# Kernel tuning notes

Hardware: AMD Instinct MI355X
Metric: run time of the kernel (lower is better)

## Reference

```python
import jax, jax.numpy as jnp
import numpy as np

B, IN, OUT = 256, 1024, 1024


def choquet_cardinal(z):
    """Discrete Choquet integral over last axis with cardinality measure mu(A)=|A|/n.
    ChI(x) = sum_i (x_(i) - x_(i-1)) * mu(A_i), x_(0)=0, mu(A_i)=(n-i+1)/n.
    """
    n = z.shape[-1]
    xs = jnp.sort(z, axis=-1)  # ascending
    # diffs[..., 0] = x_(1); diffs[..., i] = x_(i+1) - x_(i)
    diffs = jnp.concatenate([xs[..., :1], jnp.diff(xs, axis=-1)], axis=-1)
    mu = (n - jnp.arange(n, dtype=xs.dtype)) / n  # 1, (n-1)/n, ..., 1/n
    return jnp.einsum('...i,i->...', diffs, mu)


def setup_inputs() -> dict:
    key = jax.random.key(0)
    kx, kw, kb = jax.random.split(key, 3)
    x = jax.random.normal(kx, (B, 1, IN), dtype=jnp.float32)
    weight = jax.random.normal(kw, (IN, OUT), dtype=jnp.float32) * 0.02
    bias = jax.random.normal(kb, (IN, OUT), dtype=jnp.float32) * 0.02
    return {"x": x, "weight": weight, "bias": bias}


def reference(x, weight, bias):
    # z: [B, OUT, IN] = x * W^T + b^T (elementwise with broadcast)
    z = x * weight.T + bias.T
    chi = choquet_cardinal(z)  # [B, OUT]
    return jax.nn.sigmoid(chi)
```

## Files before the change

kernel.cpp:

```cpp
#include <hip/hip_runtime.h>
#include <math.h>


#define BATCH   256
#define IN_DIM  1024
#define OUT_DIM 1024

#define APACK_OFF 0
#define WPACK_OFF (512 * 1024)
#define BPART_OFF (2560 * 1024)

#define NWTASK_A   512
#define NWTASK_W  2048
#define NWTASK_B   256
#define NBLK_PREP ((NWTASK_A + NWTASK_W + NWTASK_B) / 4)

typedef __bf16 bf16x8 __attribute__((ext_vector_type(8)));
typedef float  f32x4  __attribute__((ext_vector_type(4)));

__global__ __launch_bounds__(256) void chad_prep(
    const float* __restrict__ x,
    const float* __restrict__ w,
    const float* __restrict__ bias,
    unsigned char* __restrict__ ws)
{
    __bf16* apack = (__bf16*)(ws + APACK_OFF);
    __bf16* wpack = (__bf16*)(ws + WPACK_OFF);
    float*  bpart = (float*)(ws + BPART_OFF);

    const int t    = threadIdx.x;
    const int lane = t & 63;
    const int wv   = t >> 6;
    const int g    = blockIdx.x * 4 + wv;
    const int l16  = lane & 15;
    const int quad = lane >> 4;

    if (g < NWTASK_A) {
        const int mt = g >> 5, s = g & 31;
        const float* src = x + (size_t)(mt * 16 + l16) * IN_DIM + s * 32 + quad * 8;
        const float4 v0 = *(const float4*)src;
        const float4 v1 = *(const float4*)(src + 4);
        bf16x8 o;
        o[0] = (__bf16)v0.x; o[1] = (__bf16)v0.y; o[2] = (__bf16)v0.z; o[3] = (__bf16)v0.w;
        o[4] = (__bf16)v1.x; o[5] = (__bf16)v1.y; o[6] = (__bf16)v1.z; o[7] = (__bf16)v1.w;
        *(bf16x8*)(apack + (size_t)g * 512 + lane * 8) = o;
    } else if (g < NWTASK_A + NWTASK_W) {
        const int wt = g - NWTASK_A;
        const int nt = wt >> 5, s = wt & 31;
        const float* src = w + (size_t)(s * 32 + quad * 8) * OUT_DIM + nt * 16 + l16;
        bf16x8 o;
        #pragma unroll
        for (int j = 0; j < 8; ++j) o[j] = (__bf16)src[(size_t)j * OUT_DIM];
        *(bf16x8*)(wpack + (size_t)wt * 512 + lane * 8) = o;
    } else {
        const int bt = g - NWTASK_A - NWTASK_W;
        const int rc = bt >> 4, cc = bt & 15;
        const int col = cc * 64 + lane;
        const float* src = bias + (size_t)rc * 64 * OUT_DIM + col;
        float sum = 0.f;
        #pragma unroll 8
        for (int r = 0; r < 64; ++r) sum += src[(size_t)r * OUT_DIM];
        bpart[rc * OUT_DIM + col] = sum;
    }
}

__global__ __launch_bounds__(256) void chad_gemm(
    const unsigned char* __restrict__ ws,
    float* __restrict__ out)
{
    const __bf16* apack = (const __bf16*)(ws + APACK_OFF);
    const __bf16* wpack = (const __bf16*)(ws + WPACK_OFF);
    const float*  bpart = (const float*)(ws + BPART_OFF);

    __shared__ float red[4][64][4];
    __shared__ float cs_lds[16];

    const int t    = threadIdx.x;
    const int lane = t & 63;
    const int wv   = t >> 6;
    const int mt   = blockIdx.x >> 6;
    const int nt   = blockIdx.x & 63;

    const __bf16* ab = apack + ((size_t)(mt * 32 + wv * 8) * 64 + lane) * 8;
    const __bf16* bb = wpack + ((size_t)(nt * 32 + wv * 8) * 64 + lane) * 8;

    bf16x8 af[8], bfv[8];
    #pragma unroll
    for (int i = 0; i < 8; ++i) {
        af[i]  = *(const bf16x8*)(ab + (size_t)i * 512);
        bfv[i] = *(const bf16x8*)(bb + (size_t)i * 512);
    }

    f32x4 acc = {0.f, 0.f, 0.f, 0.f};
    #pragma unroll
    for (int i = 0; i < 8; ++i)
        acc = __builtin_amdgcn_mfma_f32_16x16x32_bf16(af[i], bfv[i], acc, 0, 0, 0);

    *(f32x4*)&red[wv][lane][0] = acc;

    if (t < 16) {
        float s = 0.f;
        #pragma unroll
        for (int p = 0; p < 16; ++p) s += bpart[p * OUT_DIM + nt * 16 + t];
        cs_lds[t] = s;
    }
    __syncthreads();

    const int row = t >> 4, col = t & 15;
    const int rl  = ((row >> 2) << 4) + col;
    const int rr  = row & 3;
    float v = red[0][rl][rr] + red[1][rl][rr] + red[2][rl][rr] + red[3][rl][rr];
    v = (v + cs_lds[col]) * (1.0f / (float)IN_DIM);
    out[(size_t)(mt * 16 + row) * OUT_DIM + nt * 16 + col] = 1.0f / (1.0f + __expf(-v));
}

extern "C" void kernel_launch(void* const* d_in, const int* in_sizes, int n_in,
                              void* d_out, int out_size, void* d_ws, size_t ws_size,
                              hipStream_t stream) {
    const float* x  = (const float*)d_in[0];
    const float* w  = (const float*)d_in[1];
    const float* b  = (const float*)d_in[2];
    float* out = (float*)d_out;

    chad_prep<<<NBLK_PREP, 256, 0, stream>>>(x, w, b, (unsigned char*)d_ws);
    chad_gemm<<<(BATCH / 16) * (OUT_DIM / 16), 256, 0, stream>>>(
        (const unsigned char*)d_ws, out);
}
```

Measured before the change: 70.75 us.

## Fuse bf16 packing and bias column-sum into the MFMA kernel

Drops the separate prep kernel and workspace. The GEMM kernel now loads x and W directly from fp32, converts them to bf16 in registers, and computes the bias column sums itself. This removes a kernel launch and a round trip through the workspace. In exchange, every batch-tile block re-reads its 1024x16 slice of W and bias with strided 64-byte accesses, so that traffic is repeated 16 times and relies on cache hits.

```diff
diff --git a/kernel.cpp b/kernel.cpp
--- a/kernel.cpp
+++ b/kernel.cpp
@@ -6,103 +6,56 @@
 #define IN_DIM  1024
 #define OUT_DIM 1024
 
-#define APACK_OFF 0
-#define WPACK_OFF (512 * 1024)
-#define BPART_OFF (2560 * 1024)
-
-#define NWTASK_A   512
-#define NWTASK_W  2048
-#define NWTASK_B   256
-#define NBLK_PREP ((NWTASK_A + NWTASK_W + NWTASK_B) / 4)
-
 typedef __bf16 bf16x8 __attribute__((ext_vector_type(8)));
 typedef float  f32x4  __attribute__((ext_vector_type(4)));
 
-__global__ __launch_bounds__(256) void chad_prep(
+__global__ __launch_bounds__(256) void chad_fused(
     const float* __restrict__ x,
     const float* __restrict__ w,
     const float* __restrict__ bias,
-    unsigned char* __restrict__ ws)
+    float* __restrict__ out)
 {
-    __bf16* apack = (__bf16*)(ws + APACK_OFF);
-    __bf16* wpack = (__bf16*)(ws + WPACK_OFF);
-    float*  bpart = (float*)(ws + BPART_OFF);
+    __shared__ float red[4][64][4];
+    __shared__ float bsum[16][16];
 
     const int t    = threadIdx.x;
     const int lane = t & 63;
     const int wv   = t >> 6;
-    const int g    = blockIdx.x * 4 + wv;
     const int l16  = lane & 15;
     const int quad = lane >> 4;
-
-    if (g < NWTASK_A) {
-        const int mt = g >> 5, s = g & 31;
-        const float* src = x + (size_t)(mt * 16 + l16) * IN_DIM + s * 32 + quad * 8;
-        const float4 v0 = *(const float4*)src;
-        const float4 v1 = *(const float4*)(src + 4);
-        bf16x8 o;
-        o[0] = (__bf16)v0.x; o[1] = (__bf16)v0.y; o[2] = (__bf16)v0.z; o[3] = (__bf16)v0.w;
-        o[4] = (__bf16)v1.x; o[5] = (__bf16)v1.y; o[6] = (__bf16)v1.z; o[7] = (__bf16)v1.w;
-        *(bf16x8*)(apack + (size_t)g * 512 + lane * 8) = o;
-    } else if (g < NWTASK_A + NWTASK_W) {
-        const int wt = g - NWTASK_A;
-        const int nt = wt >> 5, s = wt & 31;
-        const float* src = w + (size_t)(s * 32 + quad * 8) * OUT_DIM + nt * 16 + l16;
-        bf16x8 o;
-        #pragma unroll
-        for (int j = 0; j < 8; ++j) o[j] = (__bf16)src[(size_t)j * OUT_DIM];
-        *(bf16x8*)(wpack + (size_t)wt * 512 + lane * 8) = o;
-    } else {
-        const int bt = g - NWTASK_A - NWTASK_W;
-        const int rc = bt >> 4, cc = bt & 15;
-        const int col = cc * 64 + lane;
-        const float* src = bias + (size_t)rc * 64 * OUT_DIM + col;
-        float sum = 0.f;
-        #pragma unroll 8
-        for (int r = 0; r < 64; ++r) sum += src[(size_t)r * OUT_DIM];
-        bpart[rc * OUT_DIM + col] = sum;
-    }
-}
-
-__global__ __launch_bounds__(256) void chad_gemm(
-    const unsigned char* __restrict__ ws,
-    float* __restrict__ out)
-{
-    const __bf16* apack = (const __bf16*)(ws + APACK_OFF);
-    const __bf16* wpack = (const __bf16*)(ws + WPACK_OFF);
-    const float*  bpart = (const float*)(ws + BPART_OFF);
-
-    __shared__ float red[4][64][4];
-    __shared__ float cs_lds[16];
-
-    const int t    = threadIdx.x;
-    const int lane = t & 63;
-    const int wv   = t >> 6;
     const int mt   = blockIdx.x >> 6;
     const int nt   = blockIdx.x & 63;
 
-    const __bf16* ab = apack + ((size_t)(mt * 32 + wv * 8) * 64 + lane) * 8;
-    const __bf16* bb = wpack + ((size_t)(nt * 32 + wv * 8) * 64 + lane) * 8;
-
-    bf16x8 af[8], bfv[8];
-    #pragma unroll
-    for (int i = 0; i < 8; ++i) {
-        af[i]  = *(const bf16x8*)(ab + (size_t)i * 512);
-        bfv[i] = *(const bf16x8*)(bb + (size_t)i * 512);
-    }
+    const float* ap = x + (size_t)(mt * 16 + l16) * IN_DIM + wv * 256 + quad * 8;
+    const float* bp = w + (size_t)(wv * 256 + quad * 8) * OUT_DIM + nt * 16 + l16;
 
     f32x4 acc = {0.f, 0.f, 0.f, 0.f};
     #pragma unroll
-    for (int i = 0; i < 8; ++i)
-        acc = __builtin_amdgcn_mfma_f32_16x16x32_bf16(af[i], bfv[i], acc, 0, 0, 0);
-
+    for (int i = 0; i < 8; ++i) {
+        const float4 a0 = *(const float4*)(ap + i * 32);
+        const float4 a1 = *(const float4*)(ap + i * 32 + 4);
+        const float* bpi = bp + (size_t)i * 32 * OUT_DIM;
+        float bv[8];
+        #pragma unroll
+        for (int j = 0; j < 8; ++j) bv[j] = bpi[(size_t)j * OUT_DIM];
+        bf16x8 af, bfv;
+        af[0] = (__bf16)a0.x; af[1] = (__bf16)a0.y;
+        af[2] = (__bf16)a0.z; af[3] = (__bf16)a0.w;
+        af[4] = (__bf16)a1.x; af[5] = (__bf16)a1.y;
+        af[6] = (__bf16)a1.z; af[7] = (__bf16)a1.w;
+        #pragma unroll
+        for (int j = 0; j < 8; ++j) bfv[j] = (__bf16)bv[j];
+        acc = __builtin_amdgcn_mfma_f32_16x16x32_bf16(af, bfv, acc, 0, 0, 0);
+    }
     *(f32x4*)&red[wv][lane][0] = acc;
 
-    if (t < 16) {
+    {
+        const int rg = t >> 4;
+        const float* bb = bias + (size_t)rg * 64 * OUT_DIM + nt * 16 + (t & 15);
         float s = 0.f;
-        #pragma unroll
-        for (int p = 0; p < 16; ++p) s += bpart[p * OUT_DIM + nt * 16 + t];
-        cs_lds[t] = s;
+        #pragma unroll 8
+        for (int r = 0; r < 64; ++r) s += bb[(size_t)r * OUT_DIM];
+        bsum[rg][t & 15] = s;
     }
     __syncthreads();
 
@@ -110,7 +63,10 @@
     const int rl  = ((row >> 2) << 4) + col;
     const int rr  = row & 3;
     float v = red[0][rl][rr] + red[1][rl][rr] + red[2][rl][rr] + red[3][rl][rr];
-    v = (v + cs_lds[col]) * (1.0f / (float)IN_DIM);
+    float cs = 0.f;
+    #pragma unroll
+    for (int p = 0; p < 16; ++p) cs += bsum[p][col];
+    v = (v + cs) * (1.0f / (float)IN_DIM);
     out[(size_t)(mt * 16 + row) * OUT_DIM + nt * 16 + col] = 1.0f / (1.0f + __expf(-v));
 }
 
@@ -120,9 +76,6 @@
     const float* x  = (const float*)d_in[0];
     const float* w  = (const float*)d_in[1];
     const float* b  = (const float*)d_in[2];
-    float* out = (float*)d_out;
-
-    chad_prep<<<NBLK_PREP, 256, 0, stream>>>(x, w, b, (unsigned char*)d_ws);
-    chad_gemm<<<(BATCH / 16) * (OUT_DIM / 16), 256, 0, stream>>>(
-        (const unsigned char*)d_ws, out);
+    chad_fused<<<(BATCH / 16) * (OUT_DIM / 16), 256, 0, stream>>>(
+        x, w, b, (float*)d_out);
 }
```

Result: slower. 77.58 us (+9.7%).
